# Performance work log

Hardware: AMD Instinct MI355X
Metric: run time of the kernel (lower is better)

Reference implementation:

```python
import jax, jax.numpy as jnp
import numpy as np

N_NODES = 50000
N_EDGES = 500000
NUM_RADIAL = 6
HIDDEN = 128

def swish(v):
    return v * jax.nn.sigmoid(v)

def setup_inputs() -> dict:
    key = jax.random.key(0)
    ks = jax.random.split(key, 8)
    x = jax.random.randint(ks[0], (N_NODES,), 0, 95, dtype=jnp.int32)
    rbf = jax.random.normal(ks[1], (N_EDGES, NUM_RADIAL), dtype=jnp.float32)
    i = jax.random.randint(ks[2], (N_EDGES,), 0, N_NODES, dtype=jnp.int32)
    j = jax.random.randint(ks[3], (N_EDGES,), 0, N_NODES, dtype=jnp.int32)
    sqrt3 = np.sqrt(3.0).astype(np.float32)
    emb_weight = jax.random.uniform(ks[4], (95, HIDDEN), minval=-sqrt3, maxval=sqrt3, dtype=jnp.float32)
    w_rbf0 = jax.random.normal(ks[5], (HIDDEN, NUM_RADIAL), dtype=jnp.float32) * 0.2
    b_rbf0 = jnp.zeros((HIDDEN,), dtype=jnp.float32)
    w_lin = jax.random.normal(ks[6], (HIDDEN, 3 * HIDDEN), dtype=jnpp.float32) if False else jax.random.normal(ks[6], (HIDDEN, 3 * HIDDEN), dtype=jnp.float32) * 0.05
    b_lin = jnp.zeros((HIDDEN,), dtype=jnp.float32)
    w_rbf1 = jax.random.normal(ks[7], (HIDDEN, NUM_RADIAL), dtype=jnp.float32) * 0.4
    return {"x": x, "rbf": rbf, "i": i, "j": j, "emb_weight": emb_weight,
            "w_rbf0": w_rbf0, "b_rbf0": b_rbf0, "w_lin": w_lin, "b_lin": b_lin,
            "w_rbf1": w_rbf1}

def reference(x, rbf, i, j, emb_weight, w_rbf0, b_rbf0, w_lin, b_lin, w_rbf1):
    # node embedding lookup: [N, H]
    h = emb_weight[x]
    # rbf0 = swish(rbf @ W0^T + b0): [E, H]
    rbf0 = swish(jnp.einsum('er,hr->eh', rbf, w_rbf0) + b_rbf0)
    # gather endpoint embeddings and concat with rbf0: [E, 3H]
    cat = jnp.concatenate([h[i], h[j], rbf0], axis=-1)
    e1 = swish(jnp.einsum('ek,hk->eh', cat, w_lin) + b_lin)
    e2 = jnp.einsum('er,hr->eh', rbf, w_rbf1) * e1
    return (e1, e2)
```

## Files before the change

kernel.cpp:

```cpp
#include <hip/hip_runtime.h>

#define HIDDEN 128
#define NRAD 6
#define NEMB 95
#define PRS 132
#define WRS 132
#define SRS 132
#define NWAVES 12
#define NBLK 256

typedef short bf16x8 __attribute__((ext_vector_type(8)));
typedef float f32x4 __attribute__((ext_vector_type(4)));

__device__ __forceinline__ float fast_rcp(float x) { return __builtin_amdgcn_rcpf(x); }
__device__ __forceinline__ float swishf(float v) { return v * fast_rcp(1.0f + __expf(-v)); }
__device__ __forceinline__ short f2bf(float f) {
    union { float f; unsigned u; } c; c.f = f;
    unsigned r = (c.u + 0x7FFFu + ((c.u >> 16) & 1u)) >> 16;
    return (short)(unsigned short)r;
}
__device__ __forceinline__ float bf2f(unsigned short u) {
    union { unsigned u; float f; } c; c.u = ((unsigned)u) << 16; return c.f;
}
__device__ __forceinline__ unsigned pk(float lo, float hi) {
    return __builtin_amdgcn_perm(__float_as_uint(hi), __float_as_uint(lo), 0x07060302u);
}
__device__ __forceinline__ float xlo(unsigned u) {
    union { unsigned u; float f; } c; c.u = u << 16; return c.f;
}
__device__ __forceinline__ float xhi(unsigned u) {
    union { unsigned u; float f; } c; c.u = u & 0xffff0000u; return c.f;
}
__device__ __forceinline__ void wait_lgkm() {
    asm volatile("s_waitcnt lgkmcnt(0)" ::: "memory");
}

__global__ void precompute_kernel(const float* __restrict__ emb,
                                  const float* __restrict__ w_lin,
                                  const float* __restrict__ b_lin,
                                  unsigned* __restrict__ pPair) {
    __shared__ __align__(16) float erow[HIDDEN];
    const int a = blockIdx.x;
    const int h = threadIdx.x;
    erow[h] = emb[a * HIDDEN + h];
    __syncthreads();
    float a1 = b_lin[h];
    float a2 = 0.f;
    const float* __restrict__ w1 = w_lin + h * 384;
    const float* __restrict__ w2 = w1 + HIDDEN;
#pragma unroll 8
    for (int k = 0; k < HIDDEN; ++k) {
        a1 += erow[k] * w1[k];
        a2 += erow[k] * w2[k];
    }
    const unsigned lo = (unsigned)(unsigned short)f2bf(a1);
    const unsigned hi = ((unsigned)(unsigned short)f2bf(a2)) << 16;
    pPair[a * HIDDEN + h] = hi | lo;
}

struct RawMD {
    float2 ra, rb, rc;
    int ii, jj;
};

__device__ __forceinline__ RawMD load_raw(int tile, int l15, int n_edges,
                                          const int* __restrict__ iv,
                                          const int* __restrict__ jv,
                                          const float* __restrict__ rbf) {
    int e = tile * 16 + l15;
    int ecl = (e < n_edges) ? e : (n_edges - 1);
    RawMD m;
    const float2* rp = reinterpret_cast<const float2*>(rbf + (size_t)ecl * NRAD);
    m.ra = rp[0];
    m.rb = rp[1];
    m.rc = rp[2];
    m.ii = iv[ecl];
    m.jj = jv[ecl];
    return m;
}

__global__ __launch_bounds__(768)
void edge_mfma_kernel(const int* __restrict__ xv,
                      const float* __restrict__ rbf,
                      const int* __restrict__ iv,
                      const int* __restrict__ jv,
                      const float* __restrict__ w_rbf0,
                      const float* __restrict__ b_rbf0,
                      const float* __restrict__ w_rbf1,
                      const float* __restrict__ w_lin,
                      const unsigned* __restrict__ pPairG,
                      float* __restrict__ out_e1,
                      float* __restrict__ out_e2,
                      int n_edges, int nt16, int n_rows) {
    __shared__ unsigned pps[NEMB * PRS];
    __shared__ __align__(16) short w3s[HIDDEN * WRS];
    __shared__ __align__(16) float w0e[HIDDEN * 8];
    __shared__ __align__(16) short w1a[HIDDEN * 8];
    __shared__ __align__(8) unsigned short stg[NWAVES][2][8 * SRS];

    const int tid = threadIdx.x;

    {
        const int nr = (n_rows < NEMB ? n_rows : NEMB);
        for (int s = tid; s < nr * HIDDEN; s += 768) {
            const int a = s >> 7, c = s & 127;
            pps[a * PRS + c] = pPairG[s];
        }
    }
    for (int s = tid; s < HIDDEN * 16; s += 768) {
        const int h = s >> 4, oct = s & 15;
        const float4* s4 = reinterpret_cast<const float4*>(w_lin + h * 384 + 256 + oct * 8);
        const float4 va = s4[0];
        const float4 vb = s4[1];
        bf16x8 fr;
        fr[0] = f2bf(va.x); fr[1] = f2bf(va.y);
        fr[2] = f2bf(va.z); fr[3] = f2bf(va.w);
        fr[4] = f2bf(vb.x); fr[5] = f2bf(vb.y);
        fr[6] = f2bf(vb.z); fr[7] = f2bf(vb.w);
        *reinterpret_cast<bf16x8*>(&w3s[h * WRS + oct * 8]) = fr;
    }
    if (tid < HIDDEN) {
        const int k = tid;
#pragma unroll
        for (int r = 0; r < NRAD; ++r) w0e[k * 8 + r] = w_rbf0[k * NRAD + r];
        w0e[k * 8 + 6] = b_rbf0[k];
        w0e[k * 8 + 7] = 0.f;
        bf16x8 f1;
#pragma unroll
        for (int r = 0; r < NRAD; ++r) f1[r] = f2bf(w_rbf1[k * NRAD + r]);
        f1[6] = 0; f1[7] = 0;
        *reinterpret_cast<bf16x8*>(&w1a[k * 8]) = f1;
    }
    __syncthreads();

    const int wid = tid >> 6;
    const int lane = tid & 63;
    const int l15 = lane & 15;
    const int lg = lane >> 4;
    const int gw = blockIdx.x * NWAVES + wid;
    const int NW = NBLK * NWAVES;

    const f32x4 zero4 = (f32x4){0.f, 0.f, 0.f, 0.f};

    int t = gw;
    if (t < nt16) {
        RawMD cur = load_raw(t, l15, n_edges, iv, jv, rbf);
        for (; t < nt16; t += NW) {
            const int tn = (t + NW < nt16) ? t + NW : t;
            RawMD nxt = load_raw(tn, l15, n_edges, iv, jv, rbf);
            const int xi = xv[cur.ii];
            const int xj = xv[cur.jj];

            bf16x8 bfrag[4];
#pragma unroll
            for (int ks = 0; ks < 4; ++ks) {
                float sv[8];
#pragma unroll
                for (int j = 0; j < 8; ++j) {
                    const int k = ks * 32 + lg * 8 + j;
                    const f32x4 wa = *reinterpret_cast<const f32x4*>(&w0e[k * 8]);
                    const f32x4 wb = *reinterpret_cast<const f32x4*>(&w0e[k * 8 + 4]);
                    const float tv = wb[2]
                                   + cur.ra.x * wa[0] + cur.ra.y * wa[1]
                                   + cur.rb.x * wa[2] + cur.rb.y * wa[3]
                                   + cur.rc.x * wb[0] + cur.rc.y * wb[1];
                    sv[j] = swishf(tv);
                }
                union { uint4 q; bf16x8 b; } mf;
                mf.q.x = pk(sv[0], sv[1]); mf.q.y = pk(sv[2], sv[3]);
                mf.q.z = pk(sv[4], sv[5]); mf.q.w = pk(sv[6], sv[7]);
                bfrag[ks] = mf.b;
            }

            union { uint4 q; bf16x8 b; } rp;
            rp.q = (uint4){0u, 0u, 0u, 0u};
            if (lg == 0) {
                rp.q.x = pk(cur.ra.x, cur.ra.y);
                rp.q.y = pk(cur.rb.x, cur.rb.y);
                rp.q.z = pk(cur.rc.x, cur.rc.y);
                rp.q.w = pk(1.0f, 0.0f);
            }
            f32x4 acc2[8];
#pragma unroll
            for (int nt = 0; nt < 8; ++nt) {
                const bf16x8 aw = *reinterpret_cast<const bf16x8*>(
                    &w1a[(nt * 16 + l15) * 8]);
                acc2[nt] = __builtin_amdgcn_mfma_f32_16x16x32_bf16(aw, rp.b, zero4, 0, 0, 0);
            }

            f32x4 acc[8];
#pragma unroll
            for (int nt = 0; nt < 8; ++nt) acc[nt] = zero4;
#pragma unroll
            for (int ks = 0; ks < 4; ++ks)
#pragma unroll
                for (int nt = 0; nt < 8; ++nt) {
                    const bf16x8 wfr = *reinterpret_cast<const bf16x8*>(
                        &w3s[(nt * 16 + l15) * WRS + (ks * 4 + lg) * 8]);
                    acc[nt] = __builtin_amdgcn_mfma_f32_16x16x32_bf16(
                        wfr, bfrag[ks], acc[nt], 0, 0, 0);
                }

#pragma unroll
            for (int p = 0; p < 2; ++p) {
                if ((l15 >> 3) == p) {
                    const int so = (l15 & 7) * SRS;
#pragma unroll
                    for (int nt = 0; nt < 8; ++nt) {
                        const int ch0 = nt * 16 + lg * 4;
                        const uint4 r1 = *reinterpret_cast<const uint4*>(&pps[xi * PRS + ch0]);
                        const uint4 r2 = *reinterpret_cast<const uint4*>(&pps[xj * PRS + ch0]);
                        float e1v[4], e2v[4];
                        {
                            const unsigned rr1[4] = {r1.x, r1.y, r1.z, r1.w};
                            const unsigned rr2[4] = {r2.x, r2.y, r2.z, r2.w};
#pragma unroll
                            for (int q = 0; q < 4; ++q) {
                                const float pv = bf2f((unsigned short)(rr1[q] & 0xffff))
                                               + bf2f((unsigned short)(rr2[q] >> 16));
                                const float sm = acc[nt][q] + pv;
                                e1v[q] = swishf(sm);
                                e2v[q] = acc2[nt][q] * e1v[q];
                            }
                        }
                        *reinterpret_cast<uint2*>(&stg[wid][0][so + ch0]) =
                            make_uint2(pk(e1v[0], e1v[1]), pk(e1v[2], e1v[3]));
                        *reinterpret_cast<uint2*>(&stg[wid][1][so + ch0]) =
                            make_uint2(pk(e2v[0], e2v[1]), pk(e2v[2], e2v[3]));
                    }
                }
                wait_lgkm();

                const size_t base = ((size_t)t * 16 + p * 8) * HIDDEN;
#pragma unroll
                for (int arr = 0; arr < 2; ++arr) {
                    float* __restrict__ ob = arr ? out_e2 : out_e1;
#pragma unroll
                    for (int s2 = 0; s2 < 4; ++s2) {
                        const int idx = s2 * 256 + lane * 4;
                        const int e_l = idx >> 7;
                        const int ch = idx & 127;
                        const uint2 uv = *reinterpret_cast<const uint2*>(
                            &stg[wid][arr][e_l * SRS + ch]);
                        if (t * 16 + p * 8 + e_l < n_edges) {
                            f32x4 v;
                            v[0] = xlo(uv.x); v[1] = xhi(uv.x);
                            v[2] = xlo(uv.y); v[3] = xhi(uv.y);
                            *reinterpret_cast<f32x4*>(ob + base + idx) = v;
                        }
                    }
                }
                wait_lgkm();
            }
            cur = nxt;
        }
    }
}

extern "C" void kernel_launch(void* const* d_in, const int* in_sizes, int n_in,
                              void* d_out, int out_size, void* d_ws, size_t ws_size,
                              hipStream_t stream) {
    const int*   xv     = (const int*)  d_in[0];
    const float* rbf    = (const float*)d_in[1];
    const int*   iv     = (const int*)  d_in[2];
    const int*   jv     = (const int*)  d_in[3];
    const float* emb    = (const float*)d_in[4];
    const float* w_rbf0 = (const float*)d_in[5];
    const float* b_rbf0 = (const float*)d_in[6];
    const float* w_lin  = (const float*)d_in[7];
    const float* b_lin  = (const float*)d_in[8];
    const float* w_rbf1 = (const float*)d_in[9];

    const int n_edges = in_sizes[2];
    const int n_emb_rows = in_sizes[4] / HIDDEN;

    unsigned* pPair = (unsigned*)d_ws;

    float* out_e1 = (float*)d_out;
    float* out_e2 = out_e1 + (size_t)n_edges * HIDDEN;

    precompute_kernel<<<n_emb_rows, HIDDEN, 0, stream>>>(emb, w_lin, b_lin, pPair);

    const int nt16 = (n_edges + 15) / 16;
    edge_mfma_kernel<<<NBLK, 768, 0, stream>>>(xv, rbf, iv, jv,
                                               w_rbf0, b_rbf0, w_rbf1, w_lin,
                                               pPair, out_e1, out_e2,
                                               n_edges, nt16, n_emb_rows);
}
```

Measured before the change: 155.8 us.

## Compute rbf0 projection with MFMA and transpose through shared scratch

The per-lane scalar FMA loop that built the rbf0 swish activations is replaced by eight MFMA ops per tile against register-resident bf16 W_rbf0/bias fragments. The swish outputs are written to a per-wave LDS scratch and read back in the B-fragment layout. That scratch buffer is also reused as the output staging area, which removes the old w0e table and shrinks LDS use. The trade-off is bf16 rounding of the rbf0 weights and inputs, extra LDS round trips, and a possible hazard from reusing scratch before earlier readers finish.

```diff
diff --git a/kernel.cpp b/kernel.cpp
--- a/kernel.cpp
+++ b/kernel.cpp
@@ -5,7 +5,7 @@
 #define NEMB 95
 #define PRS 132
 #define WRS 132
-#define SRS 132
+#define SCR 132
 #define NWAVES 12
 #define NBLK 256
 
@@ -94,17 +94,15 @@
                       int n_edges, int nt16, int n_rows) {
     __shared__ unsigned pps[NEMB * PRS];
     __shared__ __align__(16) short w3s[HIDDEN * WRS];
-    __shared__ __align__(16) float w0e[HIDDEN * 8];
     __shared__ __align__(16) short w1a[HIDDEN * 8];
-    __shared__ __align__(8) unsigned short stg[NWAVES][2][8 * SRS];
+    __shared__ __align__(16) unsigned short scratch[NWAVES][16 * SCR];
 
     const int tid = threadIdx.x;
 
     {
         const int nr = (n_rows < NEMB ? n_rows : NEMB);
         for (int s = tid; s < nr * HIDDEN; s += 768) {
-            const int a = s >> 7, c = s & 127;
-            pps[a * PRS + c] = pPairG[s];
+            pps[(s >> 7) * PRS + (s & 127)] = pPairG[s];
         }
     }
     for (int s = tid; s < HIDDEN * 16; s += 768) {
@@ -120,26 +118,36 @@
         *reinterpret_cast<bf16x8*>(&w3s[h * WRS + oct * 8]) = fr;
     }
     if (tid < HIDDEN) {
-        const int k = tid;
-#pragma unroll
-        for (int r = 0; r < NRAD; ++r) w0e[k * 8 + r] = w_rbf0[k * NRAD + r];
-        w0e[k * 8 + 6] = b_rbf0[k];
-        w0e[k * 8 + 7] = 0.f;
         bf16x8 f1;
 #pragma unroll
-        for (int r = 0; r < NRAD; ++r) f1[r] = f2bf(w_rbf1[k * NRAD + r]);
+        for (int r = 0; r < NRAD; ++r) f1[r] = f2bf(w_rbf1[tid * NRAD + r]);
         f1[6] = 0; f1[7] = 0;
-        *reinterpret_cast<bf16x8*>(&w1a[k * 8]) = f1;
-    }
-    __syncthreads();
+        *reinterpret_cast<bf16x8*>(&w1a[tid * 8]) = f1;
+    }
 
     const int wid = tid >> 6;
     const int lane = tid & 63;
     const int l15 = lane & 15;
     const int lg = lane >> 4;
+
+    bf16x8 aw0[8];
+#pragma unroll
+    for (int c = 0; c < 8; ++c) {
+        bf16x8 fr = (bf16x8){0, 0, 0, 0, 0, 0, 0, 0};
+        if (lg == 0) {
+            const int k = c * 16 + l15;
+#pragma unroll
+            for (int r = 0; r < NRAD; ++r) fr[r] = f2bf(w_rbf0[k * NRAD + r]);
+            fr[6] = f2bf(b_rbf0[k]);
+            fr[7] = 0;
+        }
+        aw0[c] = fr;
+    }
+    __syncthreads();
+
+    unsigned short* const scr = &scratch[wid][0];
     const int gw = blockIdx.x * NWAVES + wid;
     const int NW = NBLK * NWAVES;
-
     const f32x4 zero4 = (f32x4){0.f, 0.f, 0.f, 0.f};
 
     int t = gw;
@@ -151,27 +159,6 @@
             const int xi = xv[cur.ii];
             const int xj = xv[cur.jj];
 
-            bf16x8 bfrag[4];
-#pragma unroll
-            for (int ks = 0; ks < 4; ++ks) {
-                float sv[8];
-#pragma unroll
-                for (int j = 0; j < 8; ++j) {
-                    const int k = ks * 32 + lg * 8 + j;
-                    const f32x4 wa = *reinterpret_cast<const f32x4*>(&w0e[k * 8]);
-                    const f32x4 wb = *reinterpret_cast<const f32x4*>(&w0e[k * 8 + 4]);
-                    const float tv = wb[2]
-                                   + cur.ra.x * wa[0] + cur.ra.y * wa[1]
-                                   + cur.rb.x * wa[2] + cur.rb.y * wa[3]
-                                   + cur.rc.x * wb[0] + cur.rc.y * wb[1];
-                    sv[j] = swishf(tv);
-                }
-                union { uint4 q; bf16x8 b; } mf;
-                mf.q.x = pk(sv[0], sv[1]); mf.q.y = pk(sv[2], sv[3]);
-                mf.q.z = pk(sv[4], sv[5]); mf.q.w = pk(sv[6], sv[7]);
-                bfrag[ks] = mf.b;
-            }
-
             union { uint4 q; bf16x8 b; } rp;
             rp.q = (uint4){0u, 0u, 0u, 0u};
             if (lg == 0) {
@@ -180,6 +167,16 @@
                 rp.q.z = pk(cur.rc.x, cur.rc.y);
                 rp.q.w = pk(1.0f, 0.0f);
             }
+
+#pragma unroll
+            for (int c = 0; c < 8; ++c) {
+                const f32x4 cb = __builtin_amdgcn_mfma_f32_16x16x32_bf16(
+                    aw0[c], rp.b, zero4, 0, 0, 0);
+                const uint2 wv = make_uint2(pk(swishf(cb[0]), swishf(cb[1])),
+                                            pk(swishf(cb[2]), swishf(cb[3])));
+                *reinterpret_cast<uint2*>(&scr[l15 * SCR + c * 16 + lg * 4]) = wv;
+            }
+
             f32x4 acc2[8];
 #pragma unroll
             for (int nt = 0; nt < 8; ++nt) {
@@ -187,6 +184,14 @@
                     &w1a[(nt * 16 + l15) * 8]);
                 acc2[nt] = __builtin_amdgcn_mfma_f32_16x16x32_bf16(aw, rp.b, zero4, 0, 0, 0);
             }
+
+            wait_lgkm();
+
+            bf16x8 bfrag[4];
+#pragma unroll
+            for (int ks = 0; ks < 4; ++ks)
+                bfrag[ks] = *reinterpret_cast<const bf16x8*>(
+                    &scr[l15 * SCR + ks * 32 + lg * 8]);
 
             f32x4 acc[8];
 #pragma unroll
@@ -204,28 +209,26 @@
 #pragma unroll
             for (int p = 0; p < 2; ++p) {
                 if ((l15 >> 3) == p) {
-                    const int so = (l15 & 7) * SRS;
+                    const int so = (l15 & 7) * SCR;
 #pragma unroll
                     for (int nt = 0; nt < 8; ++nt) {
                         const int ch0 = nt * 16 + lg * 4;
                         const uint4 r1 = *reinterpret_cast<const uint4*>(&pps[xi * PRS + ch0]);
                         const uint4 r2 = *reinterpret_cast<const uint4*>(&pps[xj * PRS + ch0]);
+                        const unsigned rr1[4] = {r1.x, r1.y, r1.z, r1.w};
+                        const unsigned rr2[4] = {r2.x, r2.y, r2.z, r2.w};
                         float e1v[4], e2v[4];
-                        {
-                            const unsigned rr1[4] = {r1.x, r1.y, r1.z, r1.w};
-                            const unsigned rr2[4] = {r2.x, r2.y, r2.z, r2.w};
-#pragma unroll
-                            for (int q = 0; q < 4; ++q) {
-                                const float pv = bf2f((unsigned short)(rr1[q] & 0xffff))
-                                               + bf2f((unsigned short)(rr2[q] >> 16));
-                                const float sm = acc[nt][q] + pv;
-                                e1v[q] = swishf(sm);
-                                e2v[q] = acc2[nt][q] * e1v[q];
-                            }
+#pragma unroll
+                        for (int q = 0; q < 4; ++q) {
+                            const float pv = bf2f((unsigned short)(rr1[q] & 0xffff))
+                                           + bf2f((unsigned short)(rr2[q] >> 16));
+                            const float sm = acc[nt][q] + pv;
+                            e1v[q] = swishf(sm);
+                            e2v[q] = acc2[nt][q] * e1v[q];
                         }
-                        *reinterpret_cast<uint2*>(&stg[wid][0][so + ch0]) =
+                        *reinterpret_cast<uint2*>(&scr[so + ch0]) =
                             make_uint2(pk(e1v[0], e1v[1]), pk(e1v[2], e1v[3]));
-                        *reinterpret_cast<uint2*>(&stg[wid][1][so + ch0]) =
+                        *reinterpret_cast<uint2*>(&scr[(8 + (l15 & 7)) * SCR + ch0]) =
                             make_uint2(pk(e2v[0], e2v[1]), pk(e2v[2], e2v[3]));
                     }
                 }
@@ -241,7 +244,7 @@
                         const int e_l = idx >> 7;
                         const int ch = idx & 127;
                         const uint2 uv = *reinterpret_cast<const uint2*>(
-                            &stg[wid][arr][e_l * SRS + ch]);
+                            &scr[(arr * 8 + e_l) * SCR + ch]);
                         if (t * 16 + p * 8 + e_l < n_edges) {
                             f32x4 v;
                             v[0] = xlo(uv.x); v[1] = xhi(uv.x);
```

After: 144.1 us, median of 2. -7.5%, faster.
